# Optimization experiments

Measured on AMD Instinct MI355X. Metric: run time of the kernel, lower is better.

The kernel has to match this reference:

```python
import jax, jax.numpy as jnp
import numpy as np


def setup_inputs() -> dict:
    key = jax.random.key(0)
    k1, k2 = jax.random.split(key)
    B, T, D = 32, 512, 384
    x = jax.random.normal(k1, (B, T, D), dtype=jnp.float32)
    duration = jax.random.randint(k2, (B, T), 0, 8, dtype=jnp.int32)
    max_length = 4096  # T * max_duration, worst-case expanded mel length
    return {"x": x, "duration": duration, "max_length": max_length}


def reference(x, duration, max_length):
    # x: [B, T, D] float; duration: [B, T] int; returns padded expanded
    # sequence [B, M, D] and mel positions [B, M] (1-based, 0 for padding).
    B, T, D = x.shape
    cum = jnp.cumsum(duration, axis=1)          # [B, T] cumulative frame offsets
    total = cum[:, -1]                          # [B] total mel frames per batch
    frames = jnp.arange(max_length)             # [M]
    # For output frame j, source token = first i with cum[i] > j
    tok = jax.vmap(lambda c: jnp.searchsorted(c, frames, side='right'))(cum)  # [B, M]
    tok = jnp.clip(tok, 0, T - 1)
    valid = frames[None, :] < total[:, None]    # [B, M]
    out = jnp.take_along_axis(x, tok[:, :, None], axis=1)   # [B, M, D]
    out = out * valid[:, :, None].astype(x.dtype)            # zero-pad tail
    mel_pos = jnp.where(valid, frames[None, :] + 1, 0)       # [B, M]
    return out, mel_pos
```

## Files before the change

kernel.cpp:

```cpp
#include <hip/hip_runtime.h>


typedef float v4f __attribute__((ext_vector_type(4)));

constexpr int B  = 32;
constexpr int T  = 512;
constexpr int D  = 384;
constexpr int ML = 4096;
constexpr int D4 = D / 4;
constexpr int FPB = 64;
constexpr int BLOCKS_PER_BATCH = ML / FPB;
constexpr int NT = 256;
constexpr int ITERS = FPB * D4 / NT;

__global__ __launch_bounds__(NT) void lr_kernel(
        const v4f* __restrict__ x,
        const int* __restrict__ dur,
        v4f*       __restrict__ out4,
        float*     __restrict__ mel)
{
    __shared__ int s_cum[T];
    __shared__ int s_tok[FPB];
    __shared__ int s_part[NT];

    const int b      = blockIdx.x / BLOCKS_PER_BATCH;
    const int fchunk = blockIdx.x % BLOCKS_PER_BATCH;
    const int f0     = fchunk * FPB;
    const int tid    = threadIdx.x;

    const int d0 = dur[b * T + 2 * tid];
    const int d1 = dur[b * T + 2 * tid + 1];
    const int pair = d0 + d1;
    s_part[tid] = pair;
    __syncthreads();
    int val = pair;
    #pragma unroll
    for (int off = 1; off < NT; off <<= 1) {
        int t = (tid >= off) ? s_part[tid - off] : 0;
        __syncthreads();
        val += t;
        s_part[tid] = val;
        __syncthreads();
    }
    const int excl = val - pair;
    s_cum[2 * tid]     = excl + d0;
    s_cum[2 * tid + 1] = excl + pair;
    __syncthreads();
    const int total = s_cum[T - 1];

    const v4f zero4 = (v4f){0.f, 0.f, 0.f, 0.f};
    v4f* op = out4 + ((size_t)b * ML + f0) * D4 + tid;

    if (f0 >= total) {
        if (tid < FPB) mel[b * ML + f0 + tid] = 0.0f;
        #pragma unroll
        for (int k = 0; k < ITERS; ++k) {
            __builtin_nontemporal_store(zero4, op);
            op += NT;
        }
        return;
    }

    if (tid < FPB) {
        const int f = f0 + tid;
        int lo = 0, hi = T;
        while (lo < hi) {
            const int mid = (lo + hi) >> 1;
            if (s_cum[mid] <= f) lo = mid + 1; else hi = mid;
        }
        const int tok = (lo < T - 1) ? lo : (T - 1);
        s_tok[tid] = (f < total) ? tok : -1;
        mel[b * ML + f] = (f < total) ? (float)(f + 1) : 0.0f;
    }
    __syncthreads();

    const v4f* xb = x + (size_t)b * T * D4;
    int i  = tid;
    int lf = i / D4;
    int c  = i - lf * D4;
    #pragma unroll
    for (int k = 0; k < ITERS; ++k) {
        const int tok = s_tok[lf];
        v4f v = zero4;
        if (tok >= 0) v = xb[tok * D4 + c];
        __builtin_nontemporal_store(v, op);
        op += NT;
        lf += 2; c += NT - 2 * D4;
        if (c >= D4) { c -= D4; ++lf; }
    }
}

extern "C" void kernel_launch(void* const* d_in, const int* in_sizes, int n_in,
                              void* d_out, int out_size, void* d_ws, size_t ws_size,
                              hipStream_t stream) {
    const v4f* x    = (const v4f*)d_in[0];
    const int* dur  = (const int*)d_in[1];
    float* outf = (float*)d_out;
    float* mel  = outf + (size_t)B * ML * D;

    dim3 grid(B * BLOCKS_PER_BATCH);
    dim3 block(NT);
    lr_kernel<<<grid, block, 0, stream>>>(x, dur, (v4f*)outf, mel);
}
```

Baseline: 241.8 us.

## Split per-batch scan into separate kernel and remap copy blocks per XCD

Moves the cumulative-sum scan and token binary search into a separate kernel run once per batch, writing token indices, totals and mel positions to workspace. The copy kernel then reads the precomputed token indices instead of redoing the block-wide scan in every block. Copy blocks are remapped so that all chunks of one batch land on the same XCD, aiming for better L2 reuse of x rows. This costs an extra launch and a low-parallelism scan kernel with a global round-trip for the token indices.

```diff
diff --git a/kernel.cpp b/kernel.cpp
--- a/kernel.cpp
+++ b/kernel.cpp
@@ -12,21 +12,19 @@
 constexpr int BLOCKS_PER_BATCH = ML / FPB;
 constexpr int NT = 256;
 constexpr int ITERS = FPB * D4 / NT;
+constexpr int NXCD = 8;
 
-__global__ __launch_bounds__(NT) void lr_kernel(
-        const v4f* __restrict__ x,
+__global__ __launch_bounds__(NT) void lr_scan(
         const int* __restrict__ dur,
-        v4f*       __restrict__ out4,
+        int*       __restrict__ tok_ws,
+        int*       __restrict__ total_ws,
         float*     __restrict__ mel)
 {
     __shared__ int s_cum[T];
-    __shared__ int s_tok[FPB];
     __shared__ int s_part[NT];
 
-    const int b      = blockIdx.x / BLOCKS_PER_BATCH;
-    const int fchunk = blockIdx.x % BLOCKS_PER_BATCH;
-    const int f0     = fchunk * FPB;
-    const int tid    = threadIdx.x;
+    const int b   = blockIdx.x;
+    const int tid = threadIdx.x;
 
     const int d0 = dur[b * T + 2 * tid];
     const int d1 = dur[b * T + 2 * tid + 1];
@@ -47,12 +45,42 @@
     s_cum[2 * tid + 1] = excl + pair;
     __syncthreads();
     const int total = s_cum[T - 1];
+    if (tid == 0) total_ws[b] = total;
 
+    #pragma unroll
+    for (int j = 0; j < ML / NT; ++j) {
+        const int f = tid + NT * j;
+        int lo = 0, hi = T;
+        while (lo < hi) {
+            const int mid = (lo + hi) >> 1;
+            if (s_cum[mid] <= f) lo = mid + 1; else hi = mid;
+        }
+        const int tok = (lo < T - 1) ? lo : (T - 1);
+        const bool valid = f < total;
+        tok_ws[b * ML + f] = valid ? tok : -1;
+        mel[b * ML + f]    = valid ? (float)(f + 1) : 0.0f;
+    }
+}
+
+__global__ __launch_bounds__(NT) void lr_copy(
+        const v4f* __restrict__ x,
+        const int* __restrict__ tok_ws,
+        const int* __restrict__ total_ws,
+        v4f*       __restrict__ out4)
+{
+    const int i_blk  = blockIdx.x;
+    const int xcd    = i_blk & (NXCD - 1);
+    const int j      = i_blk >> 3;
+    const int b      = xcd + NXCD * (j >> 6);
+    const int fchunk = j & (BLOCKS_PER_BATCH - 1);
+    const int f0     = fchunk * FPB;
+    const int tid    = threadIdx.x;
+
+    const int total = total_ws[b];
     const v4f zero4 = (v4f){0.f, 0.f, 0.f, 0.f};
     v4f* op = out4 + ((size_t)b * ML + f0) * D4 + tid;
 
     if (f0 >= total) {
-        if (tid < FPB) mel[b * ML + f0 + tid] = 0.0f;
         #pragma unroll
         for (int k = 0; k < ITERS; ++k) {
             __builtin_nontemporal_store(zero4, op);
@@ -61,26 +89,13 @@
         return;
     }
 
-    if (tid < FPB) {
-        const int f = f0 + tid;
-        int lo = 0, hi = T;
-        while (lo < hi) {
-            const int mid = (lo + hi) >> 1;
-            if (s_cum[mid] <= f) lo = mid + 1; else hi = mid;
-        }
-        const int tok = (lo < T - 1) ? lo : (T - 1);
-        s_tok[tid] = (f < total) ? tok : -1;
-        mel[b * ML + f] = (f < total) ? (float)(f + 1) : 0.0f;
-    }
-    __syncthreads();
-
+    const int* tw = tok_ws + b * ML + f0;
     const v4f* xb = x + (size_t)b * T * D4;
-    int i  = tid;
-    int lf = i / D4;
-    int c  = i - lf * D4;
+    int lf = tid / D4;
+    int c  = tid - lf * D4;
     #pragma unroll
     for (int k = 0; k < ITERS; ++k) {
-        const int tok = s_tok[lf];
+        const int tok = tw[lf];
         v4f v = zero4;
         if (tok >= 0) v = xb[tok * D4 + c];
         __builtin_nontemporal_store(v, op);
@@ -93,12 +108,15 @@
 extern "C" void kernel_launch(void* const* d_in, const int* in_sizes, int n_in,
                               void* d_out, int out_size, void* d_ws, size_t ws_size,
                               hipStream_t stream) {
-    const v4f* x    = (const v4f*)d_in[0];
-    const int* dur  = (const int*)d_in[1];
+    const v4f* x   = (const v4f*)d_in[0];
+    const int* dur = (const int*)d_in[1];
     float* outf = (float*)d_out;
     float* mel  = outf + (size_t)B * ML * D;
 
-    dim3 grid(B * BLOCKS_PER_BATCH);
-    dim3 block(NT);
-    lr_kernel<<<grid, block, 0, stream>>>(x, dur, (v4f*)outf, mel);
+    int* tok_ws   = (int*)d_ws;
+    int* total_ws = tok_ws + (size_t)B * ML;
+
+    lr_scan<<<dim3(B), dim3(NT), 0, stream>>>(dur, tok_ws, total_ws, mel);
+    lr_copy<<<dim3(B * BLOCKS_PER_BATCH), dim3(NT), 0, stream>>>(
+        x, tok_ws, total_ws, (v4f*)outf);
 }
```

After: 248.0 us. 1.03x slower.
